# Kernel optimization log

Hardware: AMD Instinct MI355X
Metric: run time of the kernel (lower is better)

Reference implementation:

```python
import jax, jax.numpy as jnp
import numpy as np

EPS = 1e-5

def _ln(x, g, b):
    mu = jnp.mean(x, axis=-1, keepdims=True)
    var = jnp.mean(jnp.square(x - mu), axis=-1, keepdims=True)
    return (x - mu) * jax.lax.rsqrt(var + EPS) * g + b

def _mha(xq, xkv, Wq, bq, Wk, bk, Wv, bv, Wo, bo, causal):
    # Wq/Wk/Wv: [H,E,D]; per-head linear projections (no 1/sqrt(d) scaling, faithful to source)
    q = jnp.einsum('bse,hed->bhsd', xq, Wq) + bq[None, :, None, :]
    k = jnp.einsum('bte,hed->bhtd', xkv, Wk) + bk[None, :, None, :]
    v = jnp.einsum('bte,hed->bhtd', xkv, Wv) + bv[None, :, None, :]
    s = jnp.einsum('bhsd,bhtd->bhst', q, k)
    if causal:
        S, T = s.shape[-2], s.shape[-1]
        keep = jnp.tril(jnp.ones((S, T), dtype=bool))  # intended causal mask (source had inverted-mask bug -> NaNs)
        s = jnp.where(keep[None, None], s, jnp.finfo(s.dtype).min)
    w = jax.nn.softmax(s, axis=-1)
    o = jnp.einsum('bhst,bhtd->bhsd', w, v)
    B, H, S, D = o.shape
    o = o.transpose(0, 2, 1, 3).reshape(B, S, H * D)  # concat heads in order, matches torch.cat
    return o @ Wo + bo

def setup_inputs() -> dict:
    B, S, T, E, H, D, F = 4, 1024, 1024, 1024, 16, 64, 4096
    key = jax.random.key(0)
    ks = iter(jax.random.split(key, 40))
    def w(shape, scale=0.02):
        return (scale * jax.random.normal(next(ks), shape)).astype(jnp.float32)
    inp = {
        'x': w((B, S, E), 1.0),
        'enc': w((B, T, E), 1.0),
        'ln1_g': jnp.ones((E,), jnp.float32), 'ln1_b': jnp.zeros((E,), jnp.float32),
        'ln2_g': jnp.ones((E,), jnp.float32), 'ln2_b': jnp.zeros((E,), jnp.float32),
        'ln3_g': jnp.ones((E,), jnp.float32), 'ln3_b': jnp.zeros((E,), jnp.float32),
        'Wq1': w((H, E, D)), 'bq1': jnp.zeros((H, D), jnp.float32),
        'Wk1': w((H, E, D)), 'bk1': jnp.zeros((H, D), jnp.float32),
        'Wv1': w((H, E, D)), 'bv1': jnp.zeros((H, D), jnp.float32),
        'Wo1': w((E, E)), 'bo1': jnp.zeros((E,), jnp.float32),
        'Wq2': w((H, E, D)), 'bq2': jnp.zeros((H, D), jnp.float32),
        'Wk2': w((H, E, D)), 'bk2': jnp.zeros((H, D), jnp.float32),
        'Wv2': w((H, E, D)), 'bv2': jnp.zeros((H, D), jnp.float32),
        'Wo2': w((E, E)), 'bo2': jnp.zeros((E,), jnp.float32),
        'Wup': w((E, F)), 'bup': jnp.zeros((F,), jnp.float32),
        'Wdown': w((F, E)), 'bdown': jnp.zeros((E,), jnp.float32),
    }
    return inp

def reference(x, enc, ln1_g, ln1_b, ln2_g, ln2_b, ln3_g, ln3_b,
              Wq1, bq1, Wk1, bk1, Wv1, bv1, Wo1, bo1,
              Wq2, bq2, Wk2, bk2, Wv2, bv2, Wo2, bo2,
              Wup, bup, Wdown, bdown):
    h = _ln(x, ln1_g, ln1_b)
    x = x + _mha(h, h, Wq1, bq1, Wk1, bk1, Wv1, bv1, Wo1, bo1, causal=True)
    h = _ln(x, ln2_g, ln2_b)
    x = x + _mha(h, enc, Wq2, bq2, Wk2, bk2, Wv2, bv2, Wo2, bo2, causal=False)
    h = _ln(x, ln3_g, ln3_b)
    ff = jax.nn.gelu(h @ Wup + bup, approximate=False) @ Wdown + bdown  # dropout is identity in eval
    return x + ff
```

## Files before the change

kernel.cpp:

```cpp
#include <hip/hip_runtime.h>
#include <math.h>

typedef unsigned short u16;
typedef __bf16  bf16x8 __attribute__((ext_vector_type(8)));
typedef float   f32x4  __attribute__((ext_vector_type(4)));

__device__ __forceinline__ u16 f2bf(float f) {
  unsigned u = __float_as_uint(f);
  u += 0x7fffu + ((u >> 16) & 1u);
  return (u16)(u >> 16);
}
__device__ __forceinline__ void gl_lds16(const void* g, void* l) {
  __builtin_amdgcn_global_load_lds((__attribute__((address_space(1))) void*)(void*)g,
                                   (__attribute__((address_space(3))) void*)l, 16u, 0, 0u);
}
__device__ __forceinline__ f32x4 mfma16(bf16x8 a, bf16x8 b, f32x4 c) {
  return __builtin_amdgcn_mfma_f32_16x16x32_bf16(a, b, c, 0, 0, 0);
}

__global__ __launch_bounds__(256) void ln_kernel(const float* __restrict__ x,
    const float* __restrict__ g, const float* __restrict__ b, u16* __restrict__ out) {
  const long row = blockIdx.x;
  const int t = threadIdx.x;
  const float4 v = ((const float4*)(x + row * 1024))[t];
  float s  = v.x + v.y + v.z + v.w;
  float sq = v.x*v.x + v.y*v.y + v.z*v.z + v.w*v.w;
#pragma unroll
  for (int m = 1; m < 64; m <<= 1) { s += __shfl_xor(s, m); sq += __shfl_xor(sq, m); }
  __shared__ float ss[4], ssq[4];
  const int wave = t >> 6;
  if ((t & 63) == 0) { ss[wave] = s; ssq[wave] = sq; }
  __syncthreads();
  s  = ss[0] + ss[1] + ss[2] + ss[3];
  sq = ssq[0] + ssq[1] + ssq[2] + ssq[3];
  const float mu = s * (1.0f / 1024.0f);
  const float rs = rsqrtf(sq * (1.0f / 1024.0f) - mu * mu + 1e-5f);
  const float4 gg = ((const float4*)g)[t];
  const float4 bb = ((const float4*)b)[t];
  ushort4 o;
  o.x = f2bf((v.x - mu) * rs * gg.x + bb.x);
  o.y = f2bf((v.y - mu) * rs * gg.y + bb.y);
  o.z = f2bf((v.z - mu) * rs * gg.z + bb.z);
  o.w = f2bf((v.w - mu) * rs * gg.w + bb.w);
  ((ushort4*)(out + row * 1024))[t] = o;
}

__global__ __launch_bounds__(256) void cast_kernel(const float* __restrict__ in, u16* __restrict__ out) {
  const long i = ((long)blockIdx.x * 256 + threadIdx.x) * 4;
  const float4 v = *(const float4*)(in + i);
  ushort4 o;
  o.x = f2bf(v.x); o.y = f2bf(v.y); o.z = f2bf(v.z); o.w = f2bf(v.w);
  *(ushort4*)(out + i) = o;
}

__global__ __launch_bounds__(256) void tp_kernel(const float* __restrict__ in,
    u16* __restrict__ out, int C, long in_bs, long out_bs, int out_ld) {
  __shared__ u16 tile[64][65];
  in  += (long)blockIdx.z * in_bs;
  out += (long)blockIdx.z * out_bs;
  const int r0 = blockIdx.y << 6, c0 = blockIdx.x << 6;
  const int t = threadIdx.x;
  const int lr = t >> 4, lc = (t & 15) << 2;
#pragma unroll
  for (int i = 0; i < 4; i++) {
    const int row = lr + i * 16;
    const float4 v = *(const float4*)(in + (long)(r0 + row) * C + c0 + lc);
    tile[row][lc + 0] = f2bf(v.x); tile[row][lc + 1] = f2bf(v.y);
    tile[row][lc + 2] = f2bf(v.z); tile[row][lc + 3] = f2bf(v.w);
  }
  __syncthreads();
#pragma unroll
  for (int i = 0; i < 4; i++) {
    const int cc = lr + i * 16;
    ushort4 o;
    o.x = tile[lc + 0][cc]; o.y = tile[lc + 1][cc];
    o.z = tile[lc + 2][cc]; o.w = tile[lc + 3][cc];
    *(ushort4*)(out + (long)(c0 + cc) * out_ld + r0 + lc) = o;
  }
}

template<int MFRAG, int MODE>
__global__ __launch_bounds__(256, 2) void gemm_kernel(
    const u16* __restrict__ A, const u16* __restrict__ BT,
    const float* __restrict__ b0, const float* __restrict__ b1, const float* __restrict__ b2,
    const float* __restrict__ res,
    u16* __restrict__ o0, u16* __restrict__ o1, u16* __restrict__ o2,
    float* __restrict__ of, int M, int N, int K)
{
  constexpr int BM = MFRAG * 32;
  __shared__ __bf16 As[BM * 64];
  __shared__ __bf16 Bs[128 * 64];
  const int tid = threadIdx.x;
  const int wave = tid >> 6, lane = tid & 63;
  const int g = lane >> 4, li = lane & 15;
  const long m0 = (long)blockIdx.y * BM;
  const int  n0 = blockIdx.x << 7;
  const int  wr = wave >> 1, wc = wave & 1;

  f32x4 acc[MFRAG][4] = {};

  const u16* Ag = A + (m0 + wave * (MFRAG * 8) + (lane >> 3)) * K + ((lane & 7) << 3);
  const u16* Bg = BT + ((long)(n0 + wave * 32 + (lane >> 3))) * K + ((lane & 7) << 3);
  __bf16* AsW = As + wave * (MFRAG * 512);
  __bf16* BsW = Bs + wave * 2048;

  for (int k0 = 0; k0 < K; k0 += 64) {
#pragma unroll
    for (int i = 0; i < MFRAG; i++)
      gl_lds16(Ag + (long)i * 8 * K + k0, AsW + i * 512);
#pragma unroll
    for (int i = 0; i < 4; i++)
      gl_lds16(Bg + (long)i * 8 * K + k0, BsW + i * 512);
    __syncthreads();
#pragma unroll
    for (int kk = 0; kk < 2; kk++) {
      bf16x8 af[MFRAG], bv[4];
#pragma unroll
      for (int m = 0; m < MFRAG; m++)
        af[m] = *(const bf16x8*)&As[(wr * (MFRAG * 16) + m * 16 + li) * 64 + kk * 32 + g * 8];
#pragma unroll
      for (int n = 0; n < 4; n++)
        bv[n] = *(const bf16x8*)&Bs[(wc * 64 + n * 16 + li) * 64 + kk * 32 + g * 8];
#pragma unroll
      for (int m = 0; m < MFRAG; m++)
#pragma unroll
        for (int n = 0; n < 4; n++)
          acc[m][n] = mfma16(af[m], bv[n], acc[m][n]);
    }
    __syncthreads();
  }

#pragma unroll
  for (int m = 0; m < MFRAG; m++) {
#pragma unroll
    for (int n = 0; n < 4; n++) {
      const int col = n0 + wc * 64 + n * 16 + li;
#pragma unroll
      for (int r = 0; r < 4; r++) {
        const int row = (int)m0 + wr * (MFRAG * 16) + m * 16 + g * 4 + r;
        float v = acc[m][n][r];
        if constexpr (MODE == 0 || MODE == 1) {
          const int sel = col >> 10, cl = col & 1023;
          v += (MODE == 0 ? (sel == 0 ? b0 : sel == 1 ? b1 : b2)
                          : (sel == 0 ? b0 : b1))[cl];
          const int bI = row >> 10, sI = row & 1023, hI = cl >> 6, dI = cl & 63;
          const long bhI = (long)(bI * 16 + hI);
          const int qsel = (MODE == 0) ? 0 : -1;
          if (sel == qsel) {
            o0[(bhI * 1024 + sI) * 64 + dI] = f2bf(v);
          } else if (sel == qsel + 1) {
            u16* Kp = (MODE == 0) ? o1 : o0;
            Kp[(bhI * 1024 + sI) * 64 + (dI ^ ((sI & 7) << 3))] = f2bf(v);
          } else {
            u16* Vp = (MODE == 0) ? o2 : o1;
            Vp[(bhI * 64 + dI) * 1024 + (sI & ~63) + ((sI & 63) ^ ((dI & 7) << 3))] = f2bf(v);
          }
        } else if constexpr (MODE == 2) {
          v += b0[col];
          const int bI = row >> 10, sI = row & 1023, hI = col >> 6, dI = col & 63;
          o0[((long)(bI * 16 + hI) * 1024 + sI) * 64 + dI] = f2bf(v);
        } else if constexpr (MODE == 3) {
          v += b0[col];
          const long idx = (long)row * N + col;
          of[idx] = v + res[idx];
        } else {
          v += b0[col];
          const float gl = 0.5f * v * (1.0f + erff(v * 0.70710678118654752f));
          o0[(long)row * N + col] = f2bf(gl);
        }
      }
    }
  }
}

__global__ __launch_bounds__(256, 2) void attn_kernel(
    const u16* __restrict__ Q, const u16* __restrict__ Kb,
    const u16* __restrict__ VT, u16* __restrict__ O, const int causal)
{
  __shared__ u16 Ks[2][4096];
  __shared__ u16 Vs[2][4096];
  __shared__ u16 Ps[4][1024];
  const int tid = threadIdx.x;
  const int wave = tid >> 6, lane = tid & 63;
  const int g = lane >> 4, li = lane & 15;
  const int qt = blockIdx.x, bh = blockIdx.y;
  const int b_ = bh >> 4, h_ = bh & 15;
  const int q_lo = qt * 64 + wave * 16;

  const u16* Qp = Q + ((long)bh * 1024 + q_lo + li) * 64 + g * 8;
  const bf16x8 aq0 = *(const bf16x8*)Qp;
  const bf16x8 aq1 = *(const bf16x8*)(Qp + 32);

  f32x4 acc[4] = {};
  float mrun[4] = {-1e30f, -1e30f, -1e30f, -1e30f};
  float lrun[4] = {0.f, 0.f, 0.f, 0.f};

  const u16* Kbh = Kb + (long)bh * 65536;
  const u16* Vbh = VT + (long)bh * 65536;
  const int swl = (li & 7) << 3;

  const int nk = causal ? (qt + 1) : 16;

#pragma unroll
  for (int i = 0; i < 2; i++) {
    const int bc = i * 256 + wave * 64;
    gl_lds16(Kbh + (long)(bc + lane) * 8, &Ks[0][bc * 8]);
    const int ci = bc + lane, d = ci >> 3, c = ci & 7;
    gl_lds16(Vbh + (long)d * 1024 + c * 8, &Vs[0][bc * 8]);
  }
  __syncthreads();

  for (int kt = 0; kt < nk; kt++) {
    const int buf = kt & 1;
    const int k0 = kt * 64;
    if (kt + 1 < nk) {
      const int nb = buf ^ 1;
#pragma unroll
      for (int i = 0; i < 2; i++) {
        const int bc = i * 256 + wave * 64;
        gl_lds16(Kbh + (long)(kt + 1) * 4096 + (long)(bc + lane) * 8, &Ks[nb][bc * 8]);
        const int ci = bc + lane, d = ci >> 3, c = ci & 7;
        gl_lds16(Vbh + (long)d * 1024 + (kt + 1) * 64 + c * 8, &Vs[nb][bc * 8]);
      }
    }

    f32x4 s[4] = {};
#pragma unroll
    for (int n = 0; n < 4; n++) {
      const u16* kp = &Ks[buf][(n * 16 + li) * 64];
      const bf16x8 bk0 = *(const bf16x8*)(kp + ((g * 8) ^ swl));
      const bf16x8 bk1 = *(const bf16x8*)(kp + ((32 + g * 8) ^ swl));
      s[n] = mfma16(aq0, bk0, s[n]);
      s[n] = mfma16(aq1, bk1, s[n]);
    }

    if (causal && k0 + 63 > q_lo) {
#pragma unroll
      for (int n = 0; n < 4; n++) {
        const int key = k0 + n * 16 + li;
#pragma unroll
        for (int r = 0; r < 4; r++)
          if (key > q_lo + g * 4 + r) s[n][r] = -1e30f;
      }
    }

    float pmax[4];
#pragma unroll
    for (int r = 0; r < 4; r++) {
      float pm = fmaxf(fmaxf(s[0][r], s[1][r]), fmaxf(s[2][r], s[3][r]));
      pm = fmaxf(pm, __shfl_xor(pm, 1));
      pm = fmaxf(pm, __shfl_xor(pm, 2));
      pm = fmaxf(pm, __shfl_xor(pm, 4));
      pm = fmaxf(pm, __shfl_xor(pm, 8));
      pmax[r] = pm;
    }
    const bool need = (pmax[0] > mrun[0] + 8.f) || (pmax[1] > mrun[1] + 8.f) ||
                      (pmax[2] > mrun[2] + 8.f) || (pmax[3] > mrun[3] + 8.f);
    if (__any(need)) {
#pragma unroll
      for (int r = 0; r < 4; r++) {
        const float mnew = fmaxf(mrun[r], pmax[r]);
        const float sc = __expf(mrun[r] - mnew);
        mrun[r] = mnew;
        lrun[r] *= sc;
        acc[0][r] *= sc; acc[1][r] *= sc; acc[2][r] *= sc; acc[3][r] *= sc;
      }
    }
#pragma unroll
    for (int r = 0; r < 4; r++) {
      const int q = g * 4 + r;
      const int swq = (q & 7) << 3;
      const float p0 = __expf(s[0][r] - mrun[r]);
      const float p1 = __expf(s[1][r] - mrun[r]);
      const float p2 = __expf(s[2][r] - mrun[r]);
      const float p3 = __expf(s[3][r] - mrun[r]);
      u16* pw = &Ps[wave][q * 64];
      pw[(li)      ^ swq] = f2bf(p0);
      pw[(16 + li) ^ swq] = f2bf(p1);
      pw[(32 + li) ^ swq] = f2bf(p2);
      pw[(48 + li) ^ swq] = f2bf(p3);
      float rs_ = (p0 + p1) + (p2 + p3);
      rs_ += __shfl_xor(rs_, 1);
      rs_ += __shfl_xor(rs_, 2);
      rs_ += __shfl_xor(rs_, 4);
      rs_ += __shfl_xor(rs_, 8);
      lrun[r] += rs_;
    }

    const bf16x8 pa0 = *(const bf16x8*)&Ps[wave][li * 64 + ((g * 8) ^ swl)];
    const bf16x8 pa1 = *(const bf16x8*)&Ps[wave][li * 64 + ((32 + g * 8) ^ swl)];
#pragma unroll
    for (int n = 0; n < 4; n++) {
      const u16* vp = &Vs[buf][(n * 16 + li) * 64];
      const bf16x8 v0 = *(const bf16x8*)(vp + ((g * 8) ^ swl));
      const bf16x8 v1 = *(const bf16x8*)(vp + ((32 + g * 8) ^ swl));
      acc[n] = mfma16(pa0, v0, acc[n]);
      acc[n] = mfma16(pa1, v1, acc[n]);
    }
    __syncthreads();
  }

#pragma unroll
  for (int r = 0; r < 4; r++) {
    const int q = q_lo + g * 4 + r;
    const float inv = 1.0f / lrun[r];
#pragma unroll
    for (int n = 0; n < 4; n++)
      O[((long)b_ * 1024 + q) * 1024 + h_ * 64 + n * 16 + li] = f2bf(acc[n][r] * inv);
  }
}

extern "C" void kernel_launch(void* const* d_in, const int* in_sizes, int n_in,
                              void* d_out, int out_size, void* d_ws, size_t ws_size,
                              hipStream_t stream) {
  const float* x     = (const float*)d_in[0];
  const float* enc   = (const float*)d_in[1];
  const float* ln1_g = (const float*)d_in[2];
  const float* ln1_b = (const float*)d_in[3];
  const float* ln2_g = (const float*)d_in[4];
  const float* ln2_b = (const float*)d_in[5];
  const float* ln3_g = (const float*)d_in[6];
  const float* ln3_b = (const float*)d_in[7];
  const float* Wq1 = (const float*)d_in[8];  const float* bq1 = (const float*)d_in[9];
  const float* Wk1 = (const float*)d_in[10]; const float* bk1 = (const float*)d_in[11];
  const float* Wv1 = (const float*)d_in[12]; const float* bv1 = (const float*)d_in[13];
  const float* Wo1 = (const float*)d_in[14]; const float* bo1 = (const float*)d_in[15];
  const float* Wq2 = (const float*)d_in[16]; const float* bq2 = (const float*)d_in[17];
  const float* Wk2 = (const float*)d_in[18]; const float* bk2 = (const float*)d_in[19];
  const float* Wv2 = (const float*)d_in[20]; const float* bv2 = (const float*)d_in[21];
  const float* Wo2 = (const float*)d_in[22]; const float* bo2 = (const float*)d_in[23];
  const float* Wup = (const float*)d_in[24]; const float* bup = (const float*)d_in[25];
  const float* Wdn = (const float*)d_in[26]; const float* bdn = (const float*)d_in[27];

  char* ws = (char*)d_ws;
  const size_t MB = 1ull << 20;
  u16*   wpack  = (u16*)(ws);
  u16*   enc_bf = (u16*)(ws + 8 * MB);
  u16*   h_bf   = (u16*)(ws + 16 * MB);
  u16*   Qb     = (u16*)(ws + 24 * MB);
  u16*   Kbf    = (u16*)(ws + 32 * MB);
  u16*   VTb    = (u16*)(ws + 40 * MB);
  u16*   att_o  = (u16*)(ws + 48 * MB);
  float* x2     = (float*)(ws + 56 * MB);
  float* x3     = (float*)(ws + 72 * MB);
  u16*   ffmid  = (u16*)(ws + 24 * MB);

  const dim3 T(256);

  ln_kernel<<<4096, T, 0, stream>>>(x, ln1_g, ln1_b, h_bf);
  cast_kernel<<<4096, T, 0, stream>>>(enc, enc_bf);
  tp_kernel<<<dim3(1, 16, 16), T, 0, stream>>>(Wq1, wpack,               64, 65536L, 65536L, 1024);
  tp_kernel<<<dim3(1, 16, 16), T, 0, stream>>>(Wk1, wpack + 1024 * 1024, 64, 65536L, 65536L, 1024);
  tp_kernel<<<dim3(1, 16, 16), T, 0, stream>>>(Wv1, wpack + 2048 * 1024, 64, 65536L, 65536L, 1024);
  gemm_kernel<4, 0><<<dim3(24, 32), T, 0, stream>>>(h_bf, wpack, bq1, bk1, bv1, nullptr,
      Qb, Kbf, VTb, nullptr, 4096, 3072, 1024);
  attn_kernel<<<dim3(16, 64), T, 0, stream>>>(Qb, Kbf, VTb, att_o, 1);
  tp_kernel<<<dim3(16, 16, 1), T, 0, stream>>>(Wo1, wpack, 1024, 0L, 0L, 1024);
  gemm_kernel<2, 3><<<dim3(8, 64), T, 0, stream>>>(att_o, wpack, bo1, nullptr, nullptr, x,
      nullptr, nullptr, nullptr, x2, 4096, 1024, 1024);

  ln_kernel<<<4096, T, 0, stream>>>(x2, ln2_g, ln2_b, h_bf);
  tp_kernel<<<dim3(1, 16, 16), T, 0, stream>>>(Wq2, wpack, 64, 65536L, 65536L, 1024);
  gemm_kernel<2, 2><<<dim3(8, 64), T, 0, stream>>>(h_bf, wpack, bq2, nullptr, nullptr, nullptr,
      Qb, nullptr, nullptr, nullptr, 4096, 1024, 1024);
  tp_kernel<<<dim3(1, 16, 16), T, 0, stream>>>(Wk2, wpack,               64, 65536L, 65536L, 1024);
  tp_kernel<<<dim3(1, 16, 16), T, 0, stream>>>(Wv2, wpack + 1024 * 1024, 64, 65536L, 65536L, 1024);
  gemm_kernel<4, 1><<<dim3(16, 32), T, 0, stream>>>(enc_bf, wpack, bk2, bv2, nullptr, nullptr,
      Kbf, VTb, nullptr, nullptr, 4096, 2048, 1024);
  attn_kernel<<<dim3(16, 64), T, 0, stream>>>(Qb, Kbf, VTb, att_o, 0);
  tp_kernel<<<dim3(16, 16, 1), T, 0, stream>>>(Wo2, wpack, 1024, 0L, 0L, 1024);
  gemm_kernel<2, 3><<<dim3(8, 64), T, 0, stream>>>(att_o, wpack, bo2, nullptr, nullptr, x2,
      nullptr, nullptr, nullptr, x3, 4096, 1024, 1024);

  ln_kernel<<<4096, T, 0, stream>>>(x3, ln3_g, ln3_b, h_bf);
  tp_kernel<<<dim3(64, 16, 1), T, 0, stream>>>(Wup, wpack, 4096, 0L, 0L, 1024);
  gemm_kernel<4, 4><<<dim3(32, 32), T, 0, stream>>>(h_bf, wpack, bup, nullptr, nullptr, nullptr,
      ffmid, nullptr, nullptr, nullptr, 4096, 4096, 1024);
  tp_kernel<<<dim3(16, 64, 1), T, 0, stream>>>(Wdn, wpack, 1024, 0L, 0L, 4096);
  gemm_kernel<2, 3><<<dim3(8, 64), T, 0, stream>>>(ffmid, wpack, bdn, nullptr, nullptr, x3,
      nullptr, nullptr, nullptr, (float*)d_out, 4096, 1024, 4096);
}
```

Baseline: 604.1 us.

## Swizzle GEMM block order for XCD locality, merge QKV weight transposes, retile down-proj

Remaps GEMM workgroup indices so consecutive blocks, dispatched round-robin over the 8 XCDs, land on contiguous output tiles, which is meant to improve L2 reuse per XCD. Merges the three per-head Q/K/V weight transposes into one launch in each attention block, and moves the Wo transposes to a separate region so packed weights are not overwritten. Switches the FFN down-projection to a 128-row tile with half the grid. The swizzle assumes the block count is divisible by 8 and changes the tile visit order for every GEMM.

```diff
diff --git a/kernel.cpp b/kernel.cpp
--- a/kernel.cpp
+++ b/kernel.cpp
@@ -79,6 +79,33 @@
   }
 }
 
+__global__ __launch_bounds__(256) void tp3_kernel(const float* __restrict__ p0,
+    const float* __restrict__ p1, const float* __restrict__ p2, u16* __restrict__ out) {
+  __shared__ u16 tile[64][65];
+  const int z = blockIdx.z;
+  const float* in = (z < 16 ? p0 : z < 32 ? p1 : p2) + (long)(z & 15) * 65536;
+  u16* o = out + (long)z * 65536;
+  const int r0 = blockIdx.y << 6;
+  const int t = threadIdx.x;
+  const int lr = t >> 4, lc = (t & 15) << 2;
+#pragma unroll
+  for (int i = 0; i < 4; i++) {
+    const int row = lr + i * 16;
+    const float4 v = *(const float4*)(in + (long)(r0 + row) * 64 + lc);
+    tile[row][lc + 0] = f2bf(v.x); tile[row][lc + 1] = f2bf(v.y);
+    tile[row][lc + 2] = f2bf(v.z); tile[row][lc + 3] = f2bf(v.w);
+  }
+  __syncthreads();
+#pragma unroll
+  for (int i = 0; i < 4; i++) {
+    const int cc = lr + i * 16;
+    ushort4 ov;
+    ov.x = tile[lc + 0][cc]; ov.y = tile[lc + 1][cc];
+    ov.z = tile[lc + 2][cc]; ov.w = tile[lc + 3][cc];
+    *(ushort4*)(o + (long)cc * 1024 + r0 + lc) = ov;
+  }
+}
+
 template<int MFRAG, int MODE>
 __global__ __launch_bounds__(256, 2) void gemm_kernel(
     const u16* __restrict__ A, const u16* __restrict__ BT,
@@ -93,8 +120,16 @@
   const int tid = threadIdx.x;
   const int wave = tid >> 6, lane = tid & 63;
   const int g = lane >> 4, li = lane & 15;
-  const long m0 = (long)blockIdx.y * BM;
-  const int  n0 = blockIdx.x << 7;
+
+  const int gx = gridDim.x;
+  const int nwg = gx * gridDim.y;
+  const int lin = blockIdx.y * gx + blockIdx.x;
+  const int cpx = nwg >> 3;
+  const int swz = (lin & 7) * cpx + (lin >> 3);
+  const int bxs = swz % gx, bys = swz / gx;
+
+  const long m0 = (long)bys * BM;
+  const int  n0 = bxs << 7;
   const int  wr = wave >> 1, wc = wave & 1;
 
   f32x4 acc[MFRAG][4] = {};
@@ -344,32 +379,29 @@
   float* x2     = (float*)(ws + 56 * MB);
   float* x3     = (float*)(ws + 72 * MB);
   u16*   ffmid  = (u16*)(ws + 24 * MB);
+  u16*   wo_t   = wpack + 3 * 1024 * 1024;
 
   const dim3 T(256);
 
   ln_kernel<<<4096, T, 0, stream>>>(x, ln1_g, ln1_b, h_bf);
   cast_kernel<<<4096, T, 0, stream>>>(enc, enc_bf);
-  tp_kernel<<<dim3(1, 16, 16), T, 0, stream>>>(Wq1, wpack,               64, 65536L, 65536L, 1024);
-  tp_kernel<<<dim3(1, 16, 16), T, 0, stream>>>(Wk1, wpack + 1024 * 1024, 64, 65536L, 65536L, 1024);
-  tp_kernel<<<dim3(1, 16, 16), T, 0, stream>>>(Wv1, wpack + 2048 * 1024, 64, 65536L, 65536L, 1024);
+  tp3_kernel<<<dim3(1, 16, 48), T, 0, stream>>>(Wq1, Wk1, Wv1, wpack);
   gemm_kernel<4, 0><<<dim3(24, 32), T, 0, stream>>>(h_bf, wpack, bq1, bk1, bv1, nullptr,
       Qb, Kbf, VTb, nullptr, 4096, 3072, 1024);
   attn_kernel<<<dim3(16, 64), T, 0, stream>>>(Qb, Kbf, VTb, att_o, 1);
-  tp_kernel<<<dim3(16, 16, 1), T, 0, stream>>>(Wo1, wpack, 1024, 0L, 0L, 1024);
-  gemm_kernel<2, 3><<<dim3(8, 64), T, 0, stream>>>(att_o, wpack, bo1, nullptr, nullptr, x,
+  tp_kernel<<<dim3(16, 16, 1), T, 0, stream>>>(Wo1, wo_t, 1024, 0L, 0L, 1024);
+  gemm_kernel<2, 3><<<dim3(8, 64), T, 0, stream>>>(att_o, wo_t, bo1, nullptr, nullptr, x,
       nullptr, nullptr, nullptr, x2, 4096, 1024, 1024);
 
   ln_kernel<<<4096, T, 0, stream>>>(x2, ln2_g, ln2_b, h_bf);
-  tp_kernel<<<dim3(1, 16, 16), T, 0, stream>>>(Wq2, wpack, 64, 65536L, 65536L, 1024);
+  tp3_kernel<<<dim3(1, 16, 48), T, 0, stream>>>(Wq2, Wk2, Wv2, wpack);
   gemm_kernel<2, 2><<<dim3(8, 64), T, 0, stream>>>(h_bf, wpack, bq2, nullptr, nullptr, nullptr,
       Qb, nullptr, nullptr, nullptr, 4096, 1024, 1024);
-  tp_kernel<<<dim3(1, 16, 16), T, 0, stream>>>(Wk2, wpack,               64, 65536L, 65536L, 1024);
-  tp_kernel<<<dim3(1, 16, 16), T, 0, stream>>>(Wv2, wpack + 1024 * 1024, 64, 65536L, 65536L, 1024);
-  gemm_kernel<4, 1><<<dim3(16, 32), T, 0, stream>>>(enc_bf, wpack, bk2, bv2, nullptr, nullptr,
+  gemm_kernel<4, 1><<<dim3(16, 32), T, 0, stream>>>(enc_bf, wpack + 1024 * 1024, bk2, bv2, nullptr, nullptr,
       Kbf, VTb, nullptr, nullptr, 4096, 2048, 1024);
   attn_kernel<<<dim3(16, 64), T, 0, stream>>>(Qb, Kbf, VTb, att_o, 0);
-  tp_kernel<<<dim3(16, 16, 1), T, 0, stream>>>(Wo2, wpack, 1024, 0L, 0L, 1024);
-  gemm_kernel<2, 3><<<dim3(8, 64), T, 0, stream>>>(att_o, wpack, bo2, nullptr, nullptr, x2,
+  tp_kernel<<<dim3(16, 16, 1), T, 0, stream>>>(Wo2, wo_t, 1024, 0L, 0L, 1024);
+  gemm_kernel<2, 3><<<dim3(8, 64), T, 0, stream>>>(att_o, wo_t, bo2, nullptr, nullptr, x2,
       nullptr, nullptr, nullptr, x3, 4096, 1024, 1024);
 
   ln_kernel<<<4096, T, 0, stream>>>(x3, ln3_g, ln3_b, h_bf);
@@ -377,6 +409,6 @@
   gemm_kernel<4, 4><<<dim3(32, 32), T, 0, stream>>>(h_bf, wpack, bup, nullptr, nullptr, nullptr,
       ffmid, nullptr, nullptr, nullptr, 4096, 4096, 1024);
   tp_kernel<<<dim3(16, 64, 1), T, 0, stream>>>(Wdn, wpack, 1024, 0L, 0L, 4096);
-  gemm_kernel<2, 3><<<dim3(8, 64), T, 0, stream>>>(ffmid, wpack, bdn, nullptr, nullptr, x3,
+  gemm_kernel<4, 3><<<dim3(8, 32), T, 0, stream>>>(ffmid, wpack, bdn, nullptr, nullptr, x3,
       nullptr, nullptr, nullptr, (float*)d_out, 4096, 1024, 4096);
 }
```

Result: slower. 651.0 us (+7.8%).
